# Kernel tuning notes

Measured on AMD Instinct MI355X. Metric: run time of the kernel, lower is better.

The kernel has to match this reference:

```python
import jax, jax.numpy as jnp
import numpy as np

NUM_GROUPS = 32
EPS = 1e-5


def group_norm(x, scale, bias):
    b, c, h, w = x.shape
    g = NUM_GROUPS
    xg = x.reshape(b, g, c // g, h, w)
    mean = xg.mean(axis=(2, 3, 4), keepdims=True)
    var = xg.var(axis=(2, 3, 4), keepdims=True)
    xn = (xg - mean) * jax.lax.rsqrt(var + EPS)
    xn = xn.reshape(b, c, h, w)
    return xn * scale[None, :, None, None] + bias[None, :, None, None]


def conv1x1(x, w, b):
    # x: [b,c,h,w], w: [o,c], b: [o]
    return jnp.einsum('oc,bchw->bohw', w, x) + b[None, :, None, None]


def setup_inputs() -> dict:
    key = jax.random.key(0)
    ks = jax.random.split(key, 8)
    b, c, h, w = 16, 512, 32, 32
    fan = 1.0 / np.sqrt(c)
    return {
        'x': jax.random.normal(ks[0], (b, c, h, w), dtype=jnp.float32),
        'time_emb': jax.random.normal(ks[1], (b, c), dtype=jnp.float32),
        'y': jax.random.randint(ks[2], (b,), 0, 1000, dtype=jnp.int64),
        'gn_scale': jnp.ones((c,), dtype=jnp.float32),
        'gn_bias': jnp.zeros((c,), dtype=jnp.float32),
        'w_qkv': jax.random.normal(ks[3], (3 * c, c), dtype=jnp.float32) * fan,
        'b_qkv': jax.random.normal(ks[4], (3 * c,), dtype=jnp.float32) * fan,
        'w_out': jax.random.normal(ks[5], (c, c), dtype=jnp.float32) * fan,
        'b_out': jax.random.normal(ks[6], (c,), dtype=jnp.float32) * fan,
    }


def reference(x, time_emb, y, gn_scale, gn_bias, w_qkv, b_qkv, w_out, b_out):
    b, c, h, w = x.shape
    qkv = conv1x1(group_norm(x, gn_scale, gn_bias), w_qkv, b_qkv)  # [b,3c,h,w]
    q, k, v = jnp.split(qkv, 3, axis=1)
    n = h * w
    q = q.transpose(0, 2, 3, 1).reshape(b, n, c)  # [b,n,c]
    k = k.reshape(b, c, n)                        # [b,c,n]
    v = v.transpose(0, 2, 3, 1).reshape(b, n, c)  # [b,n,c]
    scores = jnp.einsum('bnc,bcm->bnm', q, k) * (c ** -0.5)  # [b,n,n]
    attn = jax.nn.softmax(scores, axis=-1)
    out = jnp.einsum('bnm,bmc->bnc', attn, v)     # [b,n,c]
    out = out.reshape(b, h, w, c).transpose(0, 3, 1, 2)
    return conv1x1(out, w_out, b_out) + x
```

## Files before the change

kernel.cpp:

```cpp
#include <hip/hip_runtime.h>
#include <hip/hip_bf16.h>

#define NB   16
#define NC   512
#define NSPA 1024
#define GN_EPS 1e-5f
#define SCL 0.044194173824159216f

typedef __bf16 bf16x8 __attribute__((ext_vector_type(8)));
typedef __bf16 bf16x4 __attribute__((ext_vector_type(4)));
typedef float  f32x4  __attribute__((ext_vector_type(4)));

typedef __attribute__((address_space(3))) void lds_t;
typedef const __attribute__((address_space(1))) void gl_t;
#define GLDS16(g, l) __builtin_amdgcn_global_load_lds((gl_t*)(g), (lds_t*)(l), 16, 0, 0)

__device__ __forceinline__ __bf16 tob(float f) { return (__bf16)f; }

__device__ __forceinline__ int xcd_swz(int cpx) {
  return (blockIdx.x & 7) * cpx + (blockIdx.x >> 3);
}

__global__ void stats_w_kernel(const float* __restrict__ x,
                               const float* __restrict__ gn_scale,
                               const float* __restrict__ gn_bias,
                               const float* __restrict__ wq,
                               const float* __restrict__ wo,
                               const float* __restrict__ bqkv,
                               float* __restrict__ coefA, float* __restrict__ coefB,
                               __bf16* __restrict__ wqT, __bf16* __restrict__ wkT,
                               __bf16* __restrict__ wvT, __bf16* __restrict__ wob,
                               float* __restrict__ rvec, float* __restrict__ bc,
                               float* __restrict__ rowsum) {
  __shared__ __align__(16) unsigned char smem[9216];
  const int id = blockIdx.x;
  const int t = threadIdx.x;
  if (id < 512) {
    const int L = (id & 7) * 64 + (id >> 3);
    const int b = L >> 5, g = L & 31;
    const float4* base = (const float4*)(x + (size_t)(b * NC + g * 16) * NSPA);
    float s = 0.f, ss = 0.f;
#pragma unroll
    for (int i = 0; i < 16; ++i) {
      float4 v = base[i * 256 + t];
      s  += (v.x + v.y) + (v.z + v.w);
      ss += (v.x * v.x + v.y * v.y) + (v.z * v.z + v.w * v.w);
    }
#pragma unroll
    for (int off = 32; off; off >>= 1) {
      s  += __shfl_xor(s, off);
      ss += __shfl_xor(ss, off);
    }
    float* red = (float*)smem;
    const int wave = t >> 6, lane = t & 63;
    if (lane == 0) { red[wave] = s; red[4 + wave] = ss; }
    __syncthreads();
    if (t < 16) {
      const float S  = red[0] + red[1] + red[2] + red[3];
      const float SS = red[4] + red[5] + red[6] + red[7];
      const float mean = S * (1.f / 16384.f);
      const float var  = SS * (1.f / 16384.f) - mean * mean;
      const float rstd = rsqrtf(var + GN_EPS);
      const int c = g * 16 + t;
      const float a = gn_scale[c] * rstd;
      coefA[b * NC + c] = a;
      coefB[b * NC + c] = gn_bias[c] - mean * a;
    }
  } else if (id < 704) {
    const int id2 = id - 512;
    const int mat = id2 >> 6, tile = id2 & 63;
    const int o0 = (tile >> 3) * 64, c0 = (tile & 7) * 64;
    __bf16* dstT = (mat == 0) ? wqT : (mat == 1) ? wkT : wvT;
    __bf16 (*l)[72] = (__bf16(*)[72])smem;
    const int orr = t >> 2, seg = (t & 3) * 16;
    const float4* src = (const float4*)(wq + (size_t)(mat * NC + o0 + orr) * NC + c0 + seg);
#pragma unroll
    for (int i = 0; i < 4; ++i) {
      float4 v = src[i];
      l[seg + i * 4 + 0][orr] = tob(v.x);
      l[seg + i * 4 + 1][orr] = tob(v.y);
      l[seg + i * 4 + 2][orr] = tob(v.z);
      l[seg + i * 4 + 3][orr] = tob(v.w);
    }
    __syncthreads();
#pragma unroll
    for (int i = 0; i < 2; ++i) {
      const int chunk = t + i * 256;
      const int row = chunk >> 3, sg = chunk & 7;
      *(bf16x8*)(dstT + (size_t)(c0 + row) * NC + o0 + sg * 8) = *(const bf16x8*)&l[row][sg * 8];
    }
  } else if (id < 768) {
    const int idx = id - 704;
#pragma unroll
    for (int i = 0; i < 4; ++i) {
      const int tt = idx * 1024 + i * 256 + t;
      float4 v = ((const float4*)wo)[tt];
      bf16x4 w;
      w[0] = tob(v.x); w[1] = tob(v.y); w[2] = tob(v.z); w[3] = tob(v.w);
      *(bf16x4*)(wob + (size_t)tt * 4) = w;
    }
  } else if (id < 776) {
    const int c0 = (id - 768) * 64;
    const int lane = t & 63, wave = t >> 6;
    const int c = c0 + lane;
    float s = 0.f;
    for (int o = wave * 128; o < wave * 128 + 128; ++o)
      s += wq[(size_t)(NC + o) * NC + c] * bqkv[o];
    float* red = (float*)smem;
    red[wave * 64 + lane] = s;
    __syncthreads();
    if (wave == 0) {
      float tot = red[lane] + red[64 + lane] + red[128 + lane] + red[192 + lane];
      rvec[c] = tot;
    }
  } else if (id < 784) {
    const int o = (id - 776) * 64 + (t >> 2);
    const int q = t & 3;
    const float4* wr = (const float4*)(wo + (size_t)o * NC + q * 128);
    const float4* bv = (const float4*)(bqkv + 2 * NC + q * 128);
    float s = 0.f;
#pragma unroll
    for (int i = 0; i < 32; ++i) {
      float4 w4 = wr[i], b4 = bv[i];
      s += (w4.x * b4.x + w4.y * b4.y) + (w4.z * b4.z + w4.w * b4.w);
    }
    s += __shfl_xor(s, 1);
    s += __shfl_xor(s, 2);
    if (q == 0) bc[o] = s;
  } else {
    float4* dst = (float4*)(rowsum + (id - 784) * 4096);
#pragma unroll
    for (int i = 0; i < 4; ++i) dst[i * 256 + t] = make_float4(0.f, 0.f, 0.f, 0.f);
  }
}

__global__ void pack_x_kernel(const float* __restrict__ x,
                              const float* __restrict__ coefA,
                              const float* __restrict__ coefB,
                              __bf16* __restrict__ xnT) {
  const int L = xcd_swz(256);
  const int b = L >> 7, rem = L & 127;
  const int c0 = (rem >> 4) * 64, n0 = (rem & 15) * 64;
  __shared__ __bf16 l[64][72];
  const int tid = threadIdx.x;
  const int cl = tid >> 2, seg = (tid & 3) * 16;
  const float ca = coefA[b * NC + c0 + cl], cb = coefB[b * NC + c0 + cl];
  const float4* src = (const float4*)(x + (size_t)(b * NC + c0 + cl) * NSPA + n0 + seg);
#pragma unroll
  for (int i = 0; i < 4; ++i) {
    float4 v = src[i];
    l[seg + i * 4 + 0][cl] = tob(v.x * ca + cb);
    l[seg + i * 4 + 1][cl] = tob(v.y * ca + cb);
    l[seg + i * 4 + 2][cl] = tob(v.z * ca + cb);
    l[seg + i * 4 + 3][cl] = tob(v.w * ca + cb);
  }
  __syncthreads();
#pragma unroll
  for (int i = 0; i < 2; ++i) {
    const int chunk = tid + i * 256;
    const int row = chunk >> 3, s = chunk & 7;
    *(bf16x8*)(xnT + (size_t)(b * NSPA + n0 + row) * NC + c0 + s * 8) =
        *(const bf16x8*)&l[row][s * 8];
  }
}

__device__ __forceinline__ void stage_pair(const __bf16* __restrict__ A, int lda,
                                           const __bf16* __restrict__ B, int ldb,
                                           int k0, __bf16* lAf, __bf16* lBf) {
  const int tid = threadIdx.x;
#pragma unroll
  for (int i = 0; i < 4; ++i) {
    const int idx = tid + i * 256;
    const int srow = idx >> 3;
    const int ss = ((idx & 7) ^ (srow & 7)) * 8;
    GLDS16(A + (size_t)srow * lda + k0 + ss, lAf + idx * 8);
    GLDS16(B + (size_t)srow * ldb + k0 + ss, lBf + idx * 8);
  }
}

__device__ __forceinline__ void gemm_core_db(const __bf16* __restrict__ A, int lda,
                                             const __bf16* __restrict__ B, int ldb,
                                             int K, __bf16 (*lA)[128][64],
                                             __bf16 (*lB)[128][64], f32x4 acc[4][4]) {
  const int tid = threadIdx.x;
  const int lane = tid & 63, wave = tid >> 6;
  const int wm = (wave >> 1) * 64, wn = (wave & 1) * 64;
  const int fr = lane & 15, fg = (lane >> 4) * 8;
  const int nt = K >> 6;

  stage_pair(A, lda, B, ldb, 0, &lA[0][0][0], &lB[0][0][0]);
  asm volatile("s_waitcnt vmcnt(0)" ::: "memory");
  __syncthreads();
  int cur = 0;
  for (int t = 0; t < nt; ++t) {
    if (t + 1 < nt)
      stage_pair(A, lda, B, ldb, (t + 1) * 64, &lA[cur ^ 1][0][0], &lB[cur ^ 1][0][0]);
    __builtin_amdgcn_s_setprio(1);
#pragma unroll
    for (int ks = 0; ks < 2; ++ks) {
      bf16x8 af[4], bfr[4];
#pragma unroll
      for (int mi = 0; mi < 4; ++mi) {
        const int r = wm + mi * 16 + fr;
        af[mi] = *(const bf16x8*)&lA[cur][r][(ks * 32 + fg) ^ ((r & 7) << 3)];
      }
#pragma unroll
      for (int ni = 0; ni < 4; ++ni) {
        const int r = wn + ni * 16 + fr;
        bfr[ni] = *(const bf16x8*)&lB[cur][r][(ks * 32 + fg) ^ ((r & 7) << 3)];
      }
#pragma unroll
      for (int mi = 0; mi < 4; ++mi)
#pragma unroll
        for (int ni = 0; ni < 4; ++ni)
          acc[mi][ni] = __builtin_amdgcn_mfma_f32_16x16x32_bf16(af[mi], bfr[ni], acc[mi][ni], 0, 0, 0);
    }
    __builtin_amdgcn_s_setprio(0);
    if (t + 1 < nt) {
      asm volatile("s_waitcnt vmcnt(0)" ::: "memory");
      __syncthreads();
      cur ^= 1;
    }
  }
}

__global__ __launch_bounds__(256, 2) void mid_kernel(
    const __bf16* __restrict__ wqT, const __bf16* __restrict__ wkT,
    const __bf16* __restrict__ wvT, const __bf16* __restrict__ wob,
    const __bf16* __restrict__ xnT, const float* __restrict__ rvec,
    __bf16* __restrict__ Aproj, float* __restrict__ R) {
  __shared__ __bf16 lA[2][128][64], lB[2][128][64];
  const int id = blockIdx.x;
  if (id < 32) {
    const bool doM = id < 16;
    const int sub = doM ? id : id - 16;
    const int mt = sub >> 2, nt2 = sub & 3;
    const __bf16* A = doM ? (wqT + (size_t)mt * 128 * NC) : (wob + (size_t)mt * 128 * NC);
    const __bf16* B = doM ? (wkT + (size_t)nt2 * 128 * NC) : (wvT + (size_t)nt2 * 128 * NC);
    f32x4 acc[4][4] = {};
    gemm_core_db(A, NC, B, NC, NC, lA, lB, acc);

    const int tid = threadIdx.x;
    const int lane = tid & 63, wave = tid >> 6;
    const int wm = (wave >> 1) * 64, wn = (wave & 1) * 64;
    const int fr = lane & 15, fq4 = (lane >> 4) * 4;
    const int mbase = (doM ? 0 : NC) + mt * 128;
#pragma unroll
    for (int mi = 0; mi < 4; ++mi) {
      const int m = mbase + wm + mi * 16 + fq4;
#pragma unroll
      for (int ni = 0; ni < 4; ++ni) {
        const int n = nt2 * 128 + wn + ni * 16 + fr;
#pragma unroll
        for (int r = 0; r < 4; ++r)
          Aproj[(size_t)(m + r) * NC + n] = tob(acc[mi][ni][r]);
      }
    }
  } else {
    const int id2 = id - 32;
    const int L = (id2 & 7) * 32 + (id2 >> 3);
    const int b = L >> 4, j0 = (L & 15) * 64;
    const int row = threadIdx.x >> 2, q = threadIdx.x & 3;
    const __bf16* src = xnT + ((size_t)(b * NSPA) + j0 + row) * NC + q * 128;
    const float* rv = rvec + q * 128;
    float s = 0.f;
#pragma unroll
    for (int i = 0; i < 16; ++i) {
      bf16x8 v = *(const bf16x8*)(src + i * 8);
#pragma unroll
      for (int e = 0; e < 8; ++e) s += (float)v[e] * rv[i * 8 + e];
    }
    s += __shfl_xor(s, 1);
    s += __shfl_xor(s, 2);
    if (q == 0) R[b * NSPA + j0 + row] = s;
  }
}

__global__ __launch_bounds__(256, 2) void proj_kernel(
    const __bf16* __restrict__ Aproj, const __bf16* __restrict__ xnT,
    const float* __restrict__ bc, __bf16* __restrict__ Yt, __bf16* __restrict__ vp) {
  const int L = xcd_swz(128);
  const int pair = L >> 3, mblk = L & 7;
  const int b = pair >> 3;
  const int n0 = (pair & 7) * 128, m0 = mblk * 128;
  __shared__ __bf16 lA[2][128][64], lB[2][128][64];
  f32x4 acc[4][4] = {};
  gemm_core_db(Aproj + (size_t)m0 * NC, NC, xnT + ((size_t)b * NSPA + n0) * NC, NC,
               NC, lA, lB, acc);

  const int lane = threadIdx.x & 63, wave = threadIdx.x >> 6;
  const int wm = (wave >> 1) * 64, wn = (wave & 1) * 64;
  const int fr = lane & 15, fq4 = (lane >> 4) * 4;
  if (m0 < NC) {
#pragma unroll
    for (int mi = 0; mi < 4; ++mi) {
      const int m = m0 + wm + mi * 16 + fq4;
#pragma unroll
      for (int ni = 0; ni < 4; ++ni) {
        const int n = n0 + wn + ni * 16 + fr;
        bf16x4 w;
        w[0] = tob(acc[mi][ni][0]);
        w[1] = tob(acc[mi][ni][1]);
        w[2] = tob(acc[mi][ni][2]);
        w[3] = tob(acc[mi][ni][3]);
        *(bf16x4*)(Yt + ((size_t)b * NSPA + n) * NC + m) = w;
      }
    }
  } else {
#pragma unroll
    for (int mi = 0; mi < 4; ++mi) {
      const int m = m0 + wm + mi * 16 + fq4;
      const int d = m - NC;
      const float4 bias = *(const float4*)(bc + d);
#pragma unroll
      for (int ni = 0; ni < 4; ++ni) {
        const int n = n0 + wn + ni * 16 + fr;
        vp[((size_t)b * NC + d + 0) * NSPA + n] = tob(acc[mi][ni][0] + bias.x);
        vp[((size_t)b * NC + d + 1) * NSPA + n] = tob(acc[mi][ni][1] + bias.y);
        vp[((size_t)b * NC + d + 2) * NSPA + n] = tob(acc[mi][ni][2] + bias.z);
        vp[((size_t)b * NC + d + 3) * NSPA + n] = tob(acc[mi][ni][3] + bias.w);
      }
    }
  }
}

__global__ __launch_bounds__(256, 2) void scores_kernel(
    const __bf16* __restrict__ Yt, const __bf16* __restrict__ xnT,
    const float* __restrict__ R, __bf16* __restrict__ P,
    float* __restrict__ rowsum) {
  const int L = xcd_swz(128);
  const int b = L >> 6, r = L & 63;
  const int i0 = (r >> 3) * 128, j0 = (r & 7) * 128;
  __shared__ __bf16 lA[2][128][64], lB[2][128][64];
  f32x4 acc[4][4] = {};
  gemm_core_db(Yt + ((size_t)b * NSPA + j0) * NC, NC,
               xnT + ((size_t)b * NSPA + i0) * NC, NC, NC, lA, lB, acc);

  const int lane = threadIdx.x & 63, wave = threadIdx.x >> 6;
  const int wm = (wave >> 1) * 64, wn = (wave & 1) * 64;
  const int fr = lane & 15, fq4 = (lane >> 4) * 4;
  float rsum[4] = {0.f, 0.f, 0.f, 0.f};
#pragma unroll
  for (int mi = 0; mi < 4; ++mi) {
    const int j = j0 + wm + mi * 16 + fq4;
    const float4 Rb = *(const float4*)(R + b * NSPA + j);
#pragma unroll
    for (int ni = 0; ni < 4; ++ni) {
      const int i = i0 + wn + ni * 16 + fr;
      bf16x4 w;
      w[0] = tob(__expf((acc[mi][ni][0] + Rb.x) * SCL));
      w[1] = tob(__expf((acc[mi][ni][1] + Rb.y) * SCL));
      w[2] = tob(__expf((acc[mi][ni][2] + Rb.z) * SCL));
      w[3] = tob(__expf((acc[mi][ni][3] + Rb.w) * SCL));
      rsum[ni] += ((float)w[0] + (float)w[1]) + ((float)w[2] + (float)w[3]);
      *(bf16x4*)(P + ((size_t)b * NSPA + i) * NSPA + j) = w;
    }
  }
#pragma unroll
  for (int ni = 0; ni < 4; ++ni) {
    rsum[ni] += __shfl_xor(rsum[ni], 16);
    rsum[ni] += __shfl_xor(rsum[ni], 32);
  }
  if (lane < 16) {
#pragma unroll
    for (int ni = 0; ni < 4; ++ni)
      atomicAdd(&rowsum[b * NSPA + i0 + wn + ni * 16 + fr], rsum[ni]);
  }
}

__global__ __launch_bounds__(256, 2) void pvout_kernel(
    const __bf16* __restrict__ vp, const __bf16* __restrict__ P,
    const float* __restrict__ rowsum, const float* __restrict__ bout,
    const float* __restrict__ x, float* __restrict__ out) {
  const int L = xcd_swz(64);
  const int b = L >> 5, r = L & 31;
  const int d0 = (r >> 3) * 128, i0 = (r & 7) * 128;
  __shared__ __bf16 lA[2][128][64], lB[2][128][64];
  f32x4 acc[4][4] = {};
  gemm_core_db(vp + ((size_t)b * NC + d0) * NSPA, NSPA,
               P + ((size_t)b * NSPA + i0) * NSPA, NSPA, NSPA, lA, lB, acc);

  const int lane = threadIdx.x & 63, wave = threadIdx.x >> 6;
  const int wm = (wave >> 1) * 64, wn = (wave & 1) * 64;
  const int fr = lane & 15, fq4 = (lane >> 4) * 4;
  float inv[4];
#pragma unroll
  for (int ni = 0; ni < 4; ++ni)
    inv[ni] = 1.f / rowsum[b * NSPA + i0 + wn + ni * 16 + fr];
#pragma unroll
  for (int mi = 0; mi < 4; ++mi) {
    const int d = d0 + wm + mi * 16 + fq4;
    const float4 bias = *(const float4*)(bout + d);
#pragma unroll
    for (int ni = 0; ni < 4; ++ni) {
      const int i = i0 + wn + ni * 16 + fr;
      const size_t ix = ((size_t)b * NC + d) * NSPA + i;
      out[ix + 0 * NSPA] = acc[mi][ni][0] * inv[ni] + bias.x + x[ix + 0 * NSPA];
      out[ix + 1 * NSPA] = acc[mi][ni][1] * inv[ni] + bias.y + x[ix + 1 * NSPA];
      out[ix + 2 * NSPA] = acc[mi][ni][2] * inv[ni] + bias.z + x[ix + 2 * NSPA];
      out[ix + 3 * NSPA] = acc[mi][ni][3] * inv[ni] + bias.w + x[ix + 3 * NSPA];
    }
  }
}

extern "C" void kernel_launch(void* const* d_in, const int* in_sizes, int n_in,
                              void* d_out, int out_size, void* d_ws, size_t ws_size,
                              hipStream_t stream) {
  const float* x        = (const float*)d_in[0];
  const float* gn_scale = (const float*)d_in[3];
  const float* gn_bias  = (const float*)d_in[4];
  const float* w_qkv    = (const float*)d_in[5];
  const float* b_qkv    = (const float*)d_in[6];
  const float* w_out    = (const float*)d_in[7];
  const float* b_out    = (const float*)d_in[8];
  float* out = (float*)d_out;

  float*  coefA  = (float*)d_ws;
  float*  coefB  = coefA + NB * NC;
  float*  rvec   = coefB + NB * NC;
  float*  bc     = rvec + NC;
  float*  R      = bc + NC;
  float*  rowsum = R + NB * NSPA;
  __bf16* wqT    = (__bf16*)(rowsum + NB * NSPA);
  __bf16* wkT    = wqT + NC * NC;
  __bf16* wvT    = wkT + NC * NC;
  __bf16* wob    = wvT + NC * NC;
  __bf16* Aproj  = wob + NC * NC;
  __bf16* xnT    = Aproj + 2 * NC * NC;
  __bf16* vp     = xnT + (size_t)NB * NSPA * NC;
  __bf16* P      = vp + (size_t)NB * NC * NSPA;
  __bf16* Yt     = (__bf16*)d_out;

  stats_w_kernel<<<dim3(788), 256, 0, stream>>>(x, gn_scale, gn_bias, w_qkv, w_out,
                                                b_qkv, coefA, coefB, wqT, wkT, wvT,
                                                wob, rvec, bc, rowsum);
  pack_x_kernel<<<dim3(2048), 256, 0, stream>>>(x, coefA, coefB, xnT);
  mid_kernel<<<dim3(288), 256, 0, stream>>>(wqT, wkT, wvT, wob, xnT, rvec, Aproj, R);
  proj_kernel<<<dim3(1024), 256, 0, stream>>>(Aproj, xnT, bc, Yt, vp);
  scores_kernel<<<dim3(1024), 256, 0, stream>>>(Yt, xnT, R, P, rowsum);
  pvout_kernel<<<dim3(512), 256, 0, stream>>>(vp, P, rowsum, b_out, x, out);
}
```

Baseline: 124.2 us.

## Replace double-buffered LDS GEMM core with single buffer for higher occupancy

The shared GEMM core drops its double-buffered LDS prefetch and loads each K tile into a single buffer, with barriers before and after compute. This halves per-block LDS use, and launch bounds rise from 2 to 4 blocks per CU. The intent is to hide memory latency through more resident waves rather than software prefetch. In exchange each block now stalls on every tile load. The explicit vmcnt wait for the async global-to-LDS copies is also gone, which may leave a race if the barrier does not wait for them.

After: 120.2 us. -3.2%, faster.

```diff
diff --git a/kernel.cpp b/kernel.cpp
--- a/kernel.cpp
+++ b/kernel.cpp
@@ -178,23 +178,19 @@
   }
 }
 
-__device__ __forceinline__ void gemm_core_db(const __bf16* __restrict__ A, int lda,
+__device__ __forceinline__ void gemm_core_sb(const __bf16* __restrict__ A, int lda,
                                              const __bf16* __restrict__ B, int ldb,
-                                             int K, __bf16 (*lA)[128][64],
-                                             __bf16 (*lB)[128][64], f32x4 acc[4][4]) {
+                                             int K, __bf16 (*lA)[64],
+                                             __bf16 (*lB)[64], f32x4 acc[4][4]) {
   const int tid = threadIdx.x;
   const int lane = tid & 63, wave = tid >> 6;
   const int wm = (wave >> 1) * 64, wn = (wave & 1) * 64;
   const int fr = lane & 15, fg = (lane >> 4) * 8;
   const int nt = K >> 6;
 
-  stage_pair(A, lda, B, ldb, 0, &lA[0][0][0], &lB[0][0][0]);
-  asm volatile("s_waitcnt vmcnt(0)" ::: "memory");
-  __syncthreads();
-  int cur = 0;
   for (int t = 0; t < nt; ++t) {
-    if (t + 1 < nt)
-      stage_pair(A, lda, B, ldb, (t + 1) * 64, &lA[cur ^ 1][0][0], &lB[cur ^ 1][0][0]);
+    stage_pair(A, lda, B, ldb, t * 64, &lA[0][0], &lB[0][0]);
+    __syncthreads();
     __builtin_amdgcn_s_setprio(1);
 #pragma unroll
     for (int ks = 0; ks < 2; ++ks) {
@@ -202,12 +198,12 @@
 #pragma unroll
       for (int mi = 0; mi < 4; ++mi) {
         const int r = wm + mi * 16 + fr;
-        af[mi] = *(const bf16x8*)&lA[cur][r][(ks * 32 + fg) ^ ((r & 7) << 3)];
+        af[mi] = *(const bf16x8*)&lA[r][(ks * 32 + fg) ^ ((r & 7) << 3)];
       }
 #pragma unroll
       for (int ni = 0; ni < 4; ++ni) {
         const int r = wn + ni * 16 + fr;
-        bfr[ni] = *(const bf16x8*)&lB[cur][r][(ks * 32 + fg) ^ ((r & 7) << 3)];
+        bfr[ni] = *(const bf16x8*)&lB[r][(ks * 32 + fg) ^ ((r & 7) << 3)];
       }
 #pragma unroll
       for (int mi = 0; mi < 4; ++mi)
@@ -216,20 +212,16 @@
           acc[mi][ni] = __builtin_amdgcn_mfma_f32_16x16x32_bf16(af[mi], bfr[ni], acc[mi][ni], 0, 0, 0);
     }
     __builtin_amdgcn_s_setprio(0);
-    if (t + 1 < nt) {
-      asm volatile("s_waitcnt vmcnt(0)" ::: "memory");
-      __syncthreads();
-      cur ^= 1;
-    }
-  }
-}
-
-__global__ __launch_bounds__(256, 2) void mid_kernel(
+    if (t + 1 < nt) __syncthreads();
+  }
+}
+
+__global__ __launch_bounds__(256, 4) void mid_kernel(
     const __bf16* __restrict__ wqT, const __bf16* __restrict__ wkT,
     const __bf16* __restrict__ wvT, const __bf16* __restrict__ wob,
     const __bf16* __restrict__ xnT, const float* __restrict__ rvec,
     __bf16* __restrict__ Aproj, float* __restrict__ R) {
-  __shared__ __bf16 lA[2][128][64], lB[2][128][64];
+  __shared__ __bf16 lA[128][64], lB[128][64];
   const int id = blockIdx.x;
   if (id < 32) {
     const bool doM = id < 16;
@@ -238,7 +230,7 @@
     const __bf16* A = doM ? (wqT + (size_t)mt * 128 * NC) : (wob + (size_t)mt * 128 * NC);
     const __bf16* B = doM ? (wkT + (size_t)nt2 * 128 * NC) : (wvT + (size_t)nt2 * 128 * NC);
     f32x4 acc[4][4] = {};
-    gemm_core_db(A, NC, B, NC, NC, lA, lB, acc);
+    gemm_core_sb(A, NC, B, NC, NC, lA, lB, acc);
 
     const int tid = threadIdx.x;
     const int lane = tid & 63, wave = tid >> 6;
@@ -276,16 +268,16 @@
   }
 }
 
-__global__ __launch_bounds__(256, 2) void proj_kernel(
+__global__ __launch_bounds__(256, 4) void proj_kernel(
     const __bf16* __restrict__ Aproj, const __bf16* __restrict__ xnT,
     const float* __restrict__ bc, __bf16* __restrict__ Yt, __bf16* __restrict__ vp) {
   const int L = xcd_swz(128);
   const int pair = L >> 3, mblk = L & 7;
   const int b = pair >> 3;
   const int n0 = (pair & 7) * 128, m0 = mblk * 128;
-  __shared__ __bf16 lA[2][128][64], lB[2][128][64];
+  __shared__ __bf16 lA[128][64], lB[128][64];
   f32x4 acc[4][4] = {};
-  gemm_core_db(Aproj + (size_t)m0 * NC, NC, xnT + ((size_t)b * NSPA + n0) * NC, NC,
+  gemm_core_sb(Aproj + (size_t)m0 * NC, NC, xnT + ((size_t)b * NSPA + n0) * NC, NC,
                NC, lA, lB, acc);
 
   const int lane = threadIdx.x & 63, wave = threadIdx.x >> 6;
@@ -324,16 +316,16 @@
   }
 }
 
-__global__ __launch_bounds__(256, 2) void scores_kernel(
+__global__ __launch_bounds__(256, 4) void scores_kernel(
     const __bf16* __restrict__ Yt, const __bf16* __restrict__ xnT,
     const float* __restrict__ R, __bf16* __restrict__ P,
     float* __restrict__ rowsum) {
   const int L = xcd_swz(128);
   const int b = L >> 6, r = L & 63;
   const int i0 = (r >> 3) * 128, j0 = (r & 7) * 128;
-  __shared__ __bf16 lA[2][128][64], lB[2][128][64];
+  __shared__ __bf16 lA[128][64], lB[128][64];
   f32x4 acc[4][4] = {};
-  gemm_core_db(Yt + ((size_t)b * NSPA + j0) * NC, NC,
+  gemm_core_sb(Yt + ((size_t)b * NSPA + j0) * NC, NC,
                xnT + ((size_t)b * NSPA + i0) * NC, NC, NC, lA, lB, acc);
 
   const int lane = threadIdx.x & 63, wave = threadIdx.x >> 6;
@@ -368,16 +360,16 @@
   }
 }
 
-__global__ __launch_bounds__(256, 2) void pvout_kernel(
+__global__ __launch_bounds__(256, 4) void pvout_kernel(
     const __bf16* __restrict__ vp, const __bf16* __restrict__ P,
     const float* __restrict__ rowsum, const float* __restrict__ bout,
     const float* __restrict__ x, float* __restrict__ out) {
   const int L = xcd_swz(64);
   const int b = L >> 5, r = L & 31;
   const int d0 = (r >> 3) * 128, i0 = (r & 7) * 128;
-  __shared__ __bf16 lA[2][128][64], lB[2][128][64];
+  __shared__ __bf16 lA[128][64], lB[128][64];
   f32x4 acc[4][4] = {};
-  gemm_core_db(vp + ((size_t)b * NC + d0) * NSPA, NSPA,
+  gemm_core_sb(vp + ((size_t)b * NC + d0) * NSPA, NSPA,
                P + ((size_t)b * NSPA + i0) * NSPA, NSPA, NSPA, lA, lB, acc);
 
   const int lane = threadIdx.x & 63, wave = threadIdx.x >> 6;
```
